# Performance work log

Measured on AMD Instinct MI355X. Metric: run time of the kernel, lower is better.

The kernel has to match this reference:

```python
import jax, jax.numpy as jnp
import numpy as np
from functools import partial

HEAD_DIM = 64
KERNEL_SIZE = 3
TOPK = KERNEL_SIZE * KERNEL_SIZE  # 9 selected keys per query
SCALE = HEAD_DIM ** (-0.5)        # note: original code DIVIDES by this scale


def setup_inputs() -> dict:
    key = jax.random.key(0)
    k1, k2, k3 = jax.random.split(key, 3)
    B, d, H, W = 4, HEAD_DIM, 96, 96
    q = jax.random.normal(k1, (B, d, H, W), dtype=jnp.float32)
    k = jax.random.normal(k2, (B, d, H, W), dtype=jnp.float32)
    v = jax.random.normal(k3, (B, d, H, W), dtype=jnp.float32)
    return {"q": q, "k": k, "v": v}


def reference(q, k, v):
    B, d, H, W = q.shape
    N = H * W
    # [B, d, H, W] -> [B, N, d]
    qf = q.reshape(B, d, N).transpose(0, 2, 1)
    kf = k.reshape(B, d, N).transpose(0, 2, 1)
    vf = v.reshape(B, d, N).transpose(0, 2, 1)
    # dense scores [B, N, N]; original divides by scale (= head_dim**-0.5)
    attn = jnp.einsum('bnd,bmd->bnm', qf, kf) / SCALE
    # top-k key selection per query
    sel, idx = jax.lax.top_k(attn, TOPK)          # [B, N, K], [B, N, K]
    w = jax.nn.softmax(sel, axis=-1)              # [B, N, K]
    # gather selected values: [B, N, K, d]
    sel_v = vf[jnp.arange(B)[:, None, None], idx]
    # weighted sum over the K selected keys
    x = jnp.einsum('bnk,bnkd->bnd', w, sel_v)     # [B, N, d]
    return x.reshape(B, H, W, d)
```

## Files before the change

### kernel.cpp

```cpp
#include <hip/hip_runtime.h>
#include <math.h>

#define HD     64
#define NPIX   9216
#define B4     4
#define NQ     (B4 * NPIX)
#define K9     9
#define SSL    8
#define ZS     16
#define KQZ    (NPIX / ZS)
#define KTL    32
#define NTG    (KQZ / KTL)
#define NTS    9
#define DGATE  13.0f
#define CAP    96

typedef __attribute__((ext_vector_type(8)))  short bf16x8;
typedef __attribute__((ext_vector_type(16))) float f32x16;
typedef unsigned short ushort_t;
typedef unsigned long long u64;

__device__ __forceinline__ ushort_t f2bf(float x) {
  unsigned u = __float_as_uint(x);
  unsigned r = (u + 0x7fffu + ((u >> 16) & 1u)) >> 16;
  return (ushort_t)r;
}

__global__ __launch_bounds__(256) void prep_kernel(
    const float* __restrict__ qg, const float* __restrict__ kg,
    const float* __restrict__ vg,
    ushort_t* __restrict__ Qbf, ushort_t* __restrict__ Kbf,
    float* __restrict__ Kt, float* __restrict__ Vt, int* __restrict__ Cnt) {
  __shared__ float Ts[64][65];
  const int b = blockIdx.y, n0 = blockIdx.x * 64, z = blockIdx.z;
  const float* src = (z == 0) ? qg : (z == 1) ? kg : vg;
  const int tid = threadIdx.x;
  if (z == 0 && b == 0) Cnt[blockIdx.x * 256 + tid] = 0;
  #pragma unroll
  for (int i = 0; i < 16; ++i) {
    const int idx = i * 256 + tid, c = idx >> 6, nl = idx & 63;
    Ts[c][nl] = src[((size_t)b * HD + c) * NPIX + n0 + nl];
  }
  __syncthreads();
  if (z == 0) {
    #pragma unroll
    for (int i = 0; i < 16; ++i) {
      const int idx = i * 256 + tid, nl = idx >> 6, d = idx & 63;
      Qbf[((size_t)b * NPIX + n0 + nl) * HD + d] = f2bf(Ts[d][nl] * 8.f);
    }
  } else if (z == 1) {
    #pragma unroll
    for (int i = 0; i < 16; ++i) {
      const int idx = i * 256 + tid, nl = idx >> 6, d = idx & 63;
      const float x = Ts[d][nl];
      const size_t o = ((size_t)b * NPIX + n0 + nl) * HD + d;
      Kbf[o] = f2bf(x); Kt[o] = x;
    }
  } else {
    #pragma unroll
    for (int i = 0; i < 16; ++i) {
      const int idx = i * 256 + tid, nl = idx >> 6, d = idx & 63;
      Vt[((size_t)b * NPIX + n0 + nl) * HD + d] = Ts[d][nl];
    }
  }
}

__device__ __forceinline__ void gl_lds16(const void* g, void* l) {
  auto gp = reinterpret_cast<const unsigned int __attribute__((address_space(1)))*>(
      reinterpret_cast<uintptr_t>(g));
  auto lp = reinterpret_cast<unsigned int __attribute__((address_space(3)))*>(
      reinterpret_cast<uintptr_t>(l));
  __builtin_amdgcn_global_load_lds(gp, lp, 16, 0, 0);
}

struct LB { u64 lo, hi; int cnt; };

__device__ __forceinline__ void flushLB(LB& b, int qi, int kbase,
                                        int* __restrict__ Cnt,
                                        unsigned* __restrict__ Cand) {
  if (b.cnt == 0) return;
  const int slot = atomicAdd(&Cnt[qi], b.cnt);
  for (int j = 0; j < b.cnt; ++j) {
    const int sh = 16 * j;
    const unsigned key = (sh < 64) ? (unsigned)((b.lo >> sh) & 0xFFFFull)
                                   : (unsigned)((b.hi >> (sh - 64)) & 0xFFFFull);
    if (slot + j < CAP)
      Cand[(size_t)qi * CAP + slot + j] = (unsigned)(kbase + (int)key);
  }
  b.lo = 0ull; b.hi = 0ull; b.cnt = 0;
}

__device__ __forceinline__ void pushLB(LB& b, unsigned key10, int qi, int kbase,
                                       int* __restrict__ Cnt,
                                       unsigned* __restrict__ Cand) {
  b.hi = (b.hi << 16) | (b.lo >> 48);
  b.lo = (b.lo << 16) | (u64)key10;
  if (++b.cnt == 8) flushLB(b, qi, kbase, Cnt, Cand);
}

__global__ __launch_bounds__(64, 4) void pass_sample(
    const ushort_t* __restrict__ Qbf, const ushort_t* __restrict__ Kbf,
    float* __restrict__ Pm) {
  __shared__ __align__(16) char SM[2][4096];

  const int l = threadIdx.x;
  const int lq = l & 31, hi = l >> 5, par = lq & 7;
  const int b = blockIdx.y, qw = blockIdx.x * 64, z = blockIdx.z;
  const int kbase = z * KTL * NTS;
  const int qi0 = b * NPIX + qw + lq;
  const int qi1 = qi0 + 32;

  bf16x8 qf0[4], qf1[4];
  {
    const size_t q0 = (size_t)qi0 * HD + hi * 8;
    const size_t q1 = (size_t)qi1 * HD + hi * 8;
    #pragma unroll
    for (int i = 0; i < 4; ++i) {
      qf0[i] = *reinterpret_cast<const bf16x8*>(Qbf + q0 + i * 16);
      qf1[i] = *reinterpret_cast<const bf16x8*>(Qbf + q1 + i * 16);
    }
  }

  const char* kB = reinterpret_cast<const char*>(Kbf + (size_t)b * NPIX * HD);
  const int sr = l >> 3, sc = l & 7;
  const int srcoff = sr * 128 + ((sc ^ sr) << 4);
  int oi[4];
  #pragma unroll
  for (int i = 0; i < 4; ++i) oi[i] = lq * 128 + (((i * 2 + hi) ^ par) << 4);

  auto stage = [&](int tile, int nb) {
    const size_t toff = ((size_t)(kbase + tile * KTL)) * 128 + srcoff;
    #pragma unroll
    for (int p = 0; p < 4; ++p)
      gl_lds16(kB + toff + p * 1024, SM[nb] + p * 1024);
  };

  float m0 = -3.4e38f, m1 = -3.4e38f;
  stage(0, 0);
  __syncthreads();

  for (int t = 0; t < NTS; ++t) {
    const int cur = t & 1;
    if (t + 1 < NTS) stage(t + 1, cur ^ 1);
    const char* kt = SM[cur];

    f32x16 a0 = {0.f,0.f,0.f,0.f,0.f,0.f,0.f,0.f,0.f,0.f,0.f,0.f,0.f,0.f,0.f,0.f};
    f32x16 a1 = {0.f,0.f,0.f,0.f,0.f,0.f,0.f,0.f,0.f,0.f,0.f,0.f,0.f,0.f,0.f,0.f};
    #pragma unroll
    for (int i = 0; i < 4; ++i) {
      const bf16x8 av = *reinterpret_cast<const bf16x8*>(kt + oi[i]);
      a0 = __builtin_amdgcn_mfma_f32_32x32x16_bf16(av, qf0[i], a0, 0, 0, 0);
      a1 = __builtin_amdgcn_mfma_f32_32x32x16_bf16(av, qf1[i], a1, 0, 0, 0);
    }
    {
      const float t0 = fmaxf(fmaxf(a0[0],  a0[1]),  a0[2]);
      const float t1 = fmaxf(fmaxf(a0[3],  a0[4]),  a0[5]);
      const float t2 = fmaxf(fmaxf(a0[6],  a0[7]),  a0[8]);
      const float t3 = fmaxf(fmaxf(a0[9],  a0[10]), a0[11]);
      const float t4 = fmaxf(fmaxf(a0[12], a0[13]), a0[14]);
      m0 = fmaxf(m0, fmaxf(fmaxf(fmaxf(t0, t1), t2),
                           fmaxf(fmaxf(t3, t4), a0[15])));
    }
    {
      const float t0 = fmaxf(fmaxf(a1[0],  a1[1]),  a1[2]);
      const float t1 = fmaxf(fmaxf(a1[3],  a1[4]),  a1[5]);
      const float t2 = fmaxf(fmaxf(a1[6],  a1[7]),  a1[8]);
      const float t3 = fmaxf(fmaxf(a1[9],  a1[10]), a1[11]);
      const float t4 = fmaxf(fmaxf(a1[12], a1[13]), a1[14]);
      m1 = fmaxf(m1, fmaxf(fmaxf(fmaxf(t0, t1), t2),
                           fmaxf(fmaxf(t3, t4), a1[15])));
    }
    __syncthreads();
  }

  m0 = fmaxf(m0, __shfl_xor(m0, 32, 64));
  m1 = fmaxf(m1, __shfl_xor(m1, 32, 64));
  if (l < 32) {
    Pm[(size_t)z * NQ + qi0] = m0;
    Pm[(size_t)z * NQ + qi1] = m1;
  }
}

__global__ __launch_bounds__(64, 4) void pass_gate(
    const ushort_t* __restrict__ Qbf, const ushort_t* __restrict__ Kbf,
    const float* __restrict__ Pm,
    int* __restrict__ Cnt, unsigned* __restrict__ Cand) {
  __shared__ __align__(16) char SM[2][4096];

  const int l = threadIdx.x;
  const int lq = l & 31, hi = l >> 5, par = lq & 7;
  const int b = blockIdx.y, qw = blockIdx.x * 64, z = blockIdx.z;
  const int kbase = z * KQZ;
  const int qi0 = b * NPIX + qw + lq;
  const int qi1 = qi0 + 32;

  bf16x8 qf0[4], qf1[4];
  {
    const size_t q0 = (size_t)qi0 * HD + hi * 8;
    const size_t q1 = (size_t)qi1 * HD + hi * 8;
    #pragma unroll
    for (int i = 0; i < 4; ++i) {
      qf0[i] = *reinterpret_cast<const bf16x8*>(Qbf + q0 + i * 16);
      qf1[i] = *reinterpret_cast<const bf16x8*>(Qbf + q1 + i * 16);
    }
  }

  float tau0 = -3.4e38f, tau1 = -3.4e38f;
  #pragma unroll
  for (int s = 0; s < SSL; ++s) {
    tau0 = fmaxf(tau0, Pm[(size_t)s * NQ + qi0]);
    tau1 = fmaxf(tau1, Pm[(size_t)s * NQ + qi1]);
  }
  float gt0 = tau0 - DGATE, gt1 = tau1 - DGATE;

  const char* kB = reinterpret_cast<const char*>(Kbf + (size_t)b * NPIX * HD);
  const int sr = l >> 3, sc = l & 7;
  const int srcoff = sr * 128 + ((sc ^ sr) << 4);
  int oi[4];
  #pragma unroll
  for (int i = 0; i < 4; ++i) oi[i] = lq * 128 + (((i * 2 + hi) ^ par) << 4);

  auto stage = [&](int tile, int nb) {
    const size_t toff = ((size_t)(kbase + tile * KTL)) * 128 + srcoff;
    #pragma unroll
    for (int p = 0; p < 4; ++p)
      gl_lds16(kB + toff + p * 1024, SM[nb] + p * 1024);
  };

  LB lb0 = {0ull, 0ull, 0}, lb1 = {0ull, 0ull, 0};

  auto chain = [&](const f32x16& a, float& gt, LB& lb, int qi, int kb) {
    const float t0 = fmaxf(fmaxf(a[0],  a[1]),  a[2]);
    const float t1 = fmaxf(fmaxf(a[3],  a[4]),  a[5]);
    const float t2 = fmaxf(fmaxf(a[6],  a[7]),  a[8]);
    const float t3 = fmaxf(fmaxf(a[9],  a[10]), a[11]);
    const float t4 = fmaxf(fmaxf(a[12], a[13]), a[14]);
    const float s16 = fmaxf(fmaxf(fmaxf(t0, t1), t2),
                            fmaxf(fmaxf(t3, t4), a[15]));
    const float old = gt;
    gt = fmaxf(old, s16 - DGATE);
    if (s16 > old) {
      #pragma unroll
      for (int e = 0; e < 16; ++e) {
        const int off = (e >> 2) * 8 + (e & 3);
        if (a[e] > gt) pushLB(lb, (unsigned)(kb + off), qi, kbase, Cnt, Cand);
      }
    }
  };

  stage(0, 0);
  __syncthreads();

  for (int t = 0; t < NTG; ++t) {
    const int cur = t & 1;
    if (t + 1 < NTG) stage(t + 1, cur ^ 1);
    const char* kt = SM[cur];

    f32x16 a0 = {0.f,0.f,0.f,0.f,0.f,0.f,0.f,0.f,0.f,0.f,0.f,0.f,0.f,0.f,0.f,0.f};
    f32x16 a1 = {0.f,0.f,0.f,0.f,0.f,0.f,0.f,0.f,0.f,0.f,0.f,0.f,0.f,0.f,0.f,0.f};
    #pragma unroll
    for (int i = 0; i < 4; ++i) {
      const bf16x8 av = *reinterpret_cast<const bf16x8*>(kt + oi[i]);
      a0 = __builtin_amdgcn_mfma_f32_32x32x16_bf16(av, qf0[i], a0, 0, 0, 0);
      a1 = __builtin_amdgcn_mfma_f32_32x32x16_bf16(av, qf1[i], a1, 0, 0, 0);
    }
    const int kb = t * KTL + 4 * hi;
    chain(a0, gt0, lb0, qi0, kb);
    chain(a1, gt1, lb1, qi1, kb);
    __syncthreads();
  }

  flushLB(lb0, qi0, kbase, Cnt, Cand);
  flushLB(lb1, qi1, kbase, Cnt, Cand);
}

__global__ __launch_bounds__(256) void merge_v(
    const unsigned* __restrict__ Cand, const int* __restrict__ Cnt,
    const float* __restrict__ qg, const float* __restrict__ Kt,
    const float* __restrict__ Vt, float* __restrict__ Og) {
  __shared__ float Qs[8][HD];
  const int tid = threadIdx.x, b = blockIdx.y;
  const int nbase = blockIdx.x * 8;

  {
    const int ql = tid >> 5, d0 = (tid & 31) * 2;
    const int n = nbase + ql;
    Qs[ql][d0]     = 8.f * qg[((size_t)b * HD + d0) * NPIX + n];
    Qs[ql][d0 + 1] = 8.f * qg[((size_t)b * HD + d0 + 1) * NPIX + n];
  }
  __syncthreads();

  const int wid = tid >> 6, lane = tid & 63;
  const int half = lane >> 5, l32 = lane & 31;
  const int ql = wid * 2 + half;
  const int n  = nbase + ql;
  const int qi = b * NPIX + n;
  const int c  = min(Cnt[qi], CAP);

  u64 p[3] = {0ull, 0ull, 0ull};
  #pragma unroll
  for (int r = 0; r < 3; ++r) {
    const int j = r * 32 + l32;
    if (j < c) {
      const int idx = (int)Cand[(size_t)qi * CAP + j];
      const float4* kr = reinterpret_cast<const float4*>(
          Kt + ((size_t)b * NPIX + idx) * HD);
      float acc = 0.f;
      #pragma unroll
      for (int u = 0; u < 16; ++u) {
        const float4 qx = *reinterpret_cast<const float4*>(&Qs[ql][u * 4]);
        const float4 kx = kr[u];
        acc = fmaf(qx.x, kx.x, acc); acc = fmaf(qx.y, kx.y, acc);
        acc = fmaf(qx.z, kx.z, acc); acc = fmaf(qx.w, kx.w, acc);
      }
      unsigned ub = __float_as_uint(acc);
      ub = (ub & 0x80000000u) ? ~ub : (ub | 0x80000000u);
      p[r] = ((u64)ub << 14) | (u64)(unsigned)(0x3FFF - idx);
    }
  }

  float mv[K9]; int mi[K9];
  #pragma unroll
  for (int r = 0; r < K9; ++r) {
    u64 bst = p[0] > p[1] ? p[0] : p[1];
    bst = bst > p[2] ? bst : p[2];
    #pragma unroll
    for (int m = 1; m < 32; m <<= 1) {
      const u64 o = __shfl_xor(bst, m, 32);
      bst = (o > bst) ? o : bst;
    }
    if (bst != 0ull) {
      #pragma unroll
      for (int s = 0; s < 3; ++s) if (p[s] == bst) p[s] = 0ull;
      const int idx = 0x3FFF - (int)(bst & 0x3FFFull);
      unsigned ub = (unsigned)(bst >> 14);
      ub = (ub & 0x80000000u) ? (ub ^ 0x80000000u) : ~ub;
      mv[r] = __uint_as_float(ub);
      mi[r] = idx;
    } else {
      mv[r] = -3.4e38f; mi[r] = 0;
    }
  }

  const float mmax = mv[0];
  float wr[K9]; float wsum = 0.f;
  #pragma unroll
  for (int r = 0; r < K9; ++r) { wr[r] = expf(mv[r] - mmax); wsum += wr[r]; }
  const float inv = 1.f / wsum;

  float2 o2 = make_float2(0.f, 0.f);
  #pragma unroll
  for (int r = 0; r < K9; ++r) {
    const float w2 = wr[r] * inv;
    const float2 v2 = *reinterpret_cast<const float2*>(
        Vt + ((size_t)b * NPIX + mi[r]) * HD + l32 * 2);
    o2.x = fmaf(w2, v2.x, o2.x);
    o2.y = fmaf(w2, v2.y, o2.y);
  }
  *reinterpret_cast<float2*>(Og + ((size_t)b * NPIX + n) * HD + l32 * 2) = o2;
}

extern "C" void kernel_launch(void* const* d_in, const int* in_sizes, int n_in,
                              void* d_out, int out_size, void* d_ws, size_t ws_size,
                              hipStream_t stream) {
  const float* q = (const float*)d_in[0];
  const float* k = (const float*)d_in[1];
  const float* v = (const float*)d_in[2];
  float* o = (float*)d_out;

  const size_t asz = (size_t)B4 * NPIX * HD;
  ushort_t* Qbf = (ushort_t*)d_ws;
  ushort_t* Kbf = Qbf + asz;
  float*    Kt  = (float*)(Kbf + asz);
  float*    Vt  = Kt + asz;
  float*    Pm  = Vt + asz;
  int*      Ct  = (int*)(Pm + (size_t)SSL * NQ);
  unsigned* Cd  = (unsigned*)(Ct + NQ);

  prep_kernel<<<dim3(NPIX / 64, B4, 3), 256, 0, stream>>>(q, k, v, Qbf, Kbf, Kt, Vt, Ct);
  pass_sample<<<dim3(NPIX / 64, B4, SSL), 64, 0, stream>>>(Qbf, Kbf, Pm);
  pass_gate<<<dim3(NPIX / 64, B4, ZS), 64, 0, stream>>>(Qbf, Kbf, Pm, Ct, Cd);
  merge_v<<<dim3(NPIX / 8, B4), 256, 0, stream>>>(Cd, Ct, q, Kt, Vt, o);
}
```

Baseline: 123.6 us.

## Share K tiles across two waves per block and enlarge key tile to 64

Both the sampling and gating passes now run two waves per block, each handling 64 queries, and they share a 64-key LDS tile that both waves stage cooperatively. The aim is to halve K global-to-LDS traffic per query and halve the number of barriers per key processed. The sample pass also changes its key window, now 9 slices of 256 keys instead of 8 slices of 288, which alters the threshold estimate for the gate. The price is larger LDS buffers and block-wide synchronization across two waves.

```diff
diff --git a/kernel.cpp b/kernel.cpp
--- a/kernel.cpp
+++ b/kernel.cpp
@@ -6,12 +6,14 @@
 #define B4     4
 #define NQ     (B4 * NPIX)
 #define K9     9
-#define SSL    8
+#define QPB    128
+#define SSL    9
+#define SKEY   256
 #define ZS     16
 #define KQZ    (NPIX / ZS)
-#define KTL    32
+#define KTL    64
 #define NTG    (KQZ / KTL)
-#define NTS    9
+#define NTS    (SKEY / KTL)
 #define DGATE  13.0f
 #define CAP    96
 
@@ -98,15 +100,17 @@
   if (++b.cnt == 8) flushLB(b, qi, kbase, Cnt, Cand);
 }
 
-__global__ __launch_bounds__(64, 4) void pass_sample(
+__global__ __launch_bounds__(128, 5) void pass_sample(
     const ushort_t* __restrict__ Qbf, const ushort_t* __restrict__ Kbf,
     float* __restrict__ Pm) {
-  __shared__ __align__(16) char SM[2][4096];
-
-  const int l = threadIdx.x;
+  __shared__ __align__(16) char SM[2][8192];
+
+  const int tid = threadIdx.x;
+  const int w = tid >> 6, l = tid & 63;
   const int lq = l & 31, hi = l >> 5, par = lq & 7;
-  const int b = blockIdx.y, qw = blockIdx.x * 64, z = blockIdx.z;
-  const int kbase = z * KTL * NTS;
+  const int b = blockIdx.y, qbase = blockIdx.x * QPB, z = blockIdx.z;
+  const int kbase = z * SKEY;
+  const int qw = qbase + w * 64;
   const int qi0 = b * NPIX + qw + lq;
   const int qi1 = qi0 + 32;
 
@@ -122,8 +126,9 @@
   }
 
   const char* kB = reinterpret_cast<const char*>(Kbf + (size_t)b * NPIX * HD);
-  const int sr = l >> 3, sc = l & 7;
-  const int srcoff = sr * 128 + ((sc ^ sr) << 4);
+  const int sr = tid >> 3, sc = tid & 7;
+  const int srcoff = sr * 128 + ((sc ^ (sr & 7)) << 4);
+  const int hdst = w * 1024;
   int oi[4];
   #pragma unroll
   for (int i = 0; i < 4; ++i) oi[i] = lq * 128 + (((i * 2 + hi) ^ par) << 4);
@@ -132,7 +137,7 @@
     const size_t toff = ((size_t)(kbase + tile * KTL)) * 128 + srcoff;
     #pragma unroll
     for (int p = 0; p < 4; ++p)
-      gl_lds16(kB + toff + p * 1024, SM[nb] + p * 1024);
+      gl_lds16(kB + toff + p * 2048, SM[nb] + p * 2048 + hdst);
   };
 
   float m0 = -3.4e38f, m1 = -3.4e38f;
@@ -144,31 +149,35 @@
     if (t + 1 < NTS) stage(t + 1, cur ^ 1);
     const char* kt = SM[cur];
 
-    f32x16 a0 = {0.f,0.f,0.f,0.f,0.f,0.f,0.f,0.f,0.f,0.f,0.f,0.f,0.f,0.f,0.f,0.f};
-    f32x16 a1 = {0.f,0.f,0.f,0.f,0.f,0.f,0.f,0.f,0.f,0.f,0.f,0.f,0.f,0.f,0.f,0.f};
-    #pragma unroll
-    for (int i = 0; i < 4; ++i) {
-      const bf16x8 av = *reinterpret_cast<const bf16x8*>(kt + oi[i]);
-      a0 = __builtin_amdgcn_mfma_f32_32x32x16_bf16(av, qf0[i], a0, 0, 0, 0);
-      a1 = __builtin_amdgcn_mfma_f32_32x32x16_bf16(av, qf1[i], a1, 0, 0, 0);
-    }
-    {
-      const float t0 = fmaxf(fmaxf(a0[0],  a0[1]),  a0[2]);
-      const float t1 = fmaxf(fmaxf(a0[3],  a0[4]),  a0[5]);
-      const float t2 = fmaxf(fmaxf(a0[6],  a0[7]),  a0[8]);
-      const float t3 = fmaxf(fmaxf(a0[9],  a0[10]), a0[11]);
-      const float t4 = fmaxf(fmaxf(a0[12], a0[13]), a0[14]);
-      m0 = fmaxf(m0, fmaxf(fmaxf(fmaxf(t0, t1), t2),
-                           fmaxf(fmaxf(t3, t4), a0[15])));
-    }
-    {
-      const float t0 = fmaxf(fmaxf(a1[0],  a1[1]),  a1[2]);
-      const float t1 = fmaxf(fmaxf(a1[3],  a1[4]),  a1[5]);
-      const float t2 = fmaxf(fmaxf(a1[6],  a1[7]),  a1[8]);
-      const float t3 = fmaxf(fmaxf(a1[9],  a1[10]), a1[11]);
-      const float t4 = fmaxf(fmaxf(a1[12], a1[13]), a1[14]);
-      m1 = fmaxf(m1, fmaxf(fmaxf(fmaxf(t0, t1), t2),
-                           fmaxf(fmaxf(t3, t4), a1[15])));
+    #pragma unroll
+    for (int g = 0; g < 2; ++g) {
+      const char* kg2 = kt + g * 4096;
+      f32x16 a0 = {0.f,0.f,0.f,0.f,0.f,0.f,0.f,0.f,0.f,0.f,0.f,0.f,0.f,0.f,0.f,0.f};
+      f32x16 a1 = a0;
+      #pragma unroll
+      for (int i = 0; i < 4; ++i) {
+        const bf16x8 av = *reinterpret_cast<const bf16x8*>(kg2 + oi[i]);
+        a0 = __builtin_amdgcn_mfma_f32_32x32x16_bf16(av, qf0[i], a0, 0, 0, 0);
+        a1 = __builtin_amdgcn_mfma_f32_32x32x16_bf16(av, qf1[i], a1, 0, 0, 0);
+      }
+      {
+        const float t0 = fmaxf(fmaxf(a0[0],  a0[1]),  a0[2]);
+        const float t1 = fmaxf(fmaxf(a0[3],  a0[4]),  a0[5]);
+        const float t2 = fmaxf(fmaxf(a0[6],  a0[7]),  a0[8]);
+        const float t3 = fmaxf(fmaxf(a0[9],  a0[10]), a0[11]);
+        const float t4 = fmaxf(fmaxf(a0[12], a0[13]), a0[14]);
+        m0 = fmaxf(m0, fmaxf(fmaxf(fmaxf(t0, t1), t2),
+                             fmaxf(fmaxf(t3, t4), a0[15])));
+      }
+      {
+        const float t0 = fmaxf(fmaxf(a1[0],  a1[1]),  a1[2]);
+        const float t1 = fmaxf(fmaxf(a1[3],  a1[4]),  a1[5]);
+        const float t2 = fmaxf(fmaxf(a1[6],  a1[7]),  a1[8]);
+        const float t3 = fmaxf(fmaxf(a1[9],  a1[10]), a1[11]);
+        const float t4 = fmaxf(fmaxf(a1[12], a1[13]), a1[14]);
+        m1 = fmaxf(m1, fmaxf(fmaxf(fmaxf(t0, t1), t2),
+                             fmaxf(fmaxf(t3, t4), a1[15])));
+      }
     }
     __syncthreads();
   }
@@ -181,16 +190,18 @@
   }
 }
 
-__global__ __launch_bounds__(64, 4) void pass_gate(
+__global__ __launch_bounds__(128, 5) void pass_gate(
     const ushort_t* __restrict__ Qbf, const ushort_t* __restrict__ Kbf,
     const float* __restrict__ Pm,
     int* __restrict__ Cnt, unsigned* __restrict__ Cand) {
-  __shared__ __align__(16) char SM[2][4096];
-
-  const int l = threadIdx.x;
+  __shared__ __align__(16) char SM[2][8192];
+
+  const int tid = threadIdx.x;
+  const int w = tid >> 6, l = tid & 63;
   const int lq = l & 31, hi = l >> 5, par = lq & 7;
-  const int b = blockIdx.y, qw = blockIdx.x * 64, z = blockIdx.z;
+  const int b = blockIdx.y, qbase = blockIdx.x * QPB, z = blockIdx.z;
   const int kbase = z * KQZ;
+  const int qw = qbase + w * 64;
   const int qi0 = b * NPIX + qw + lq;
   const int qi1 = qi0 + 32;
 
@@ -214,8 +225,9 @@
   float gt0 = tau0 - DGATE, gt1 = tau1 - DGATE;
 
   const char* kB = reinterpret_cast<const char*>(Kbf + (size_t)b * NPIX * HD);
-  const int sr = l >> 3, sc = l & 7;
-  const int srcoff = sr * 128 + ((sc ^ sr) << 4);
+  const int sr = tid >> 3, sc = tid & 7;
+  const int srcoff = sr * 128 + ((sc ^ (sr & 7)) << 4);
+  const int hdst = w * 1024;
   int oi[4];
   #pragma unroll
   for (int i = 0; i < 4; ++i) oi[i] = lq * 128 + (((i * 2 + hi) ^ par) << 4);
@@ -224,12 +236,12 @@
     const size_t toff = ((size_t)(kbase + tile * KTL)) * 128 + srcoff;
     #pragma unroll
     for (int p = 0; p < 4; ++p)
-      gl_lds16(kB + toff + p * 1024, SM[nb] + p * 1024);
+      gl_lds16(kB + toff + p * 2048, SM[nb] + p * 2048 + hdst);
   };
 
   LB lb0 = {0ull, 0ull, 0}, lb1 = {0ull, 0ull, 0};
 
-  auto chain = [&](const f32x16& a, float& gt, LB& lb, int qi, int kb) {
+  auto chain = [&](const f32x16& a, float& gtc, LB& lb, int qq, int kb) {
     const float t0 = fmaxf(fmaxf(a[0],  a[1]),  a[2]);
     const float t1 = fmaxf(fmaxf(a[3],  a[4]),  a[5]);
     const float t2 = fmaxf(fmaxf(a[6],  a[7]),  a[8]);
@@ -237,13 +249,13 @@
     const float t4 = fmaxf(fmaxf(a[12], a[13]), a[14]);
     const float s16 = fmaxf(fmaxf(fmaxf(t0, t1), t2),
                             fmaxf(fmaxf(t3, t4), a[15]));
-    const float old = gt;
-    gt = fmaxf(old, s16 - DGATE);
+    const float old = gtc;
+    gtc = fmaxf(old, s16 - DGATE);
     if (s16 > old) {
       #pragma unroll
       for (int e = 0; e < 16; ++e) {
         const int off = (e >> 2) * 8 + (e & 3);
-        if (a[e] > gt) pushLB(lb, (unsigned)(kb + off), qi, kbase, Cnt, Cand);
+        if (a[e] > gtc) pushLB(lb, (unsigned)(kb + off), qq, kbase, Cnt, Cand);
       }
     }
   };
@@ -256,17 +268,21 @@
     if (t + 1 < NTG) stage(t + 1, cur ^ 1);
     const char* kt = SM[cur];
 
-    f32x16 a0 = {0.f,0.f,0.f,0.f,0.f,0.f,0.f,0.f,0.f,0.f,0.f,0.f,0.f,0.f,0.f,0.f};
-    f32x16 a1 = {0.f,0.f,0.f,0.f,0.f,0.f,0.f,0.f,0.f,0.f,0.f,0.f,0.f,0.f,0.f,0.f};
-    #pragma unroll
-    for (int i = 0; i < 4; ++i) {
-      const bf16x8 av = *reinterpret_cast<const bf16x8*>(kt + oi[i]);
-      a0 = __builtin_amdgcn_mfma_f32_32x32x16_bf16(av, qf0[i], a0, 0, 0, 0);
-      a1 = __builtin_amdgcn_mfma_f32_32x32x16_bf16(av, qf1[i], a1, 0, 0, 0);
-    }
-    const int kb = t * KTL + 4 * hi;
-    chain(a0, gt0, lb0, qi0, kb);
-    chain(a1, gt1, lb1, qi1, kb);
+    #pragma unroll
+    for (int g = 0; g < 2; ++g) {
+      const char* kg2 = kt + g * 4096;
+      f32x16 a0 = {0.f,0.f,0.f,0.f,0.f,0.f,0.f,0.f,0.f,0.f,0.f,0.f,0.f,0.f,0.f,0.f};
+      f32x16 a1 = a0;
+      #pragma unroll
+      for (int i = 0; i < 4; ++i) {
+        const bf16x8 av = *reinterpret_cast<const bf16x8*>(kg2 + oi[i]);
+        a0 = __builtin_amdgcn_mfma_f32_32x32x16_bf16(av, qf0[i], a0, 0, 0, 0);
+        a1 = __builtin_amdgcn_mfma_f32_32x32x16_bf16(av, qf1[i], a1, 0, 0, 0);
+      }
+      const int kb = t * KTL + g * 32 + 4 * hi;
+      chain(a0, gt0, lb0, qi0, kb);
+      chain(a1, gt1, lb1, qi1, kb);
+    }
     __syncthreads();
   }
 
@@ -378,7 +394,7 @@
   unsigned* Cd  = (unsigned*)(Ct + NQ);
 
   prep_kernel<<<dim3(NPIX / 64, B4, 3), 256, 0, stream>>>(q, k, v, Qbf, Kbf, Kt, Vt, Ct);
-  pass_sample<<<dim3(NPIX / 64, B4, SSL), 64, 0, stream>>>(Qbf, Kbf, Pm);
-  pass_gate<<<dim3(NPIX / 64, B4, ZS), 64, 0, stream>>>(Qbf, Kbf, Pm, Ct, Cd);
+  pass_sample<<<dim3(NPIX / QPB, B4, SSL), 128, 0, stream>>>(Qbf, Kbf, Pm);
+  pass_gate<<<dim3(NPIX / QPB, B4, ZS), 128, 0, stream>>>(Qbf, Kbf, Pm, Ct, Cd);
   merge_v<<<dim3(NPIX / 8, B4), 256, 0, stream>>>(Cd, Ct, q, Kt, Vt, o);
 }
```

Result: slower. 142.4 us (+15.3%).
